# Optimization experiments

Hardware: AMD Instinct MI355X
Metric: run time of the kernel (lower is better)

Reference implementation:

```python
import jax, jax.numpy as jnp
import numpy as np

W_DIM, T_DIM = 300, 100
IN = W_DIM + T_DIM        # 400, also LSTM hidden size
H = IN                    # hiddenSize
BI = 2 * H                # 800, biLSTM output per step
MLP_IN = 2 * BI           # 1600
VOCAB, NTAGS = 50000, 50
SEQ = 320


def _lstm_dir(xs, w_ih, w_hh, b_ih, b_hh, h0, c0, reverse):
    # xs: [T, d_in]; PyTorch gate order i, f, g, o
    if reverse:
        xs = xs[::-1]
    def step(carry, x):
        h, c = carry
        g = x @ w_ih.T + h @ w_hh.T + b_ih + b_hh
        i, f, gc, o = jnp.split(g, 4)
        i, f, o = jax.nn.sigmoid(i), jax.nn.sigmoid(f), jax.nn.sigmoid(o)
        c = f * c + i * jnp.tanh(gc)
        h = o * jnp.tanh(c)
        return (h, c), h
    _, ys = jax.lax.scan(step, (h0, c0), xs)
    return ys[::-1] if reverse else ys


def _bilstm(x, params, h0, c0):
    # x: [T, IN]; h0/c0: [4, H] ordered (l0 fwd, l0 bwd, l1 fwd, l1 bwd)
    out = x
    for layer in range(2):
        p_f = params[layer][0]
        p_b = params[layer][1]
        yf = _lstm_dir(out, *p_f, h0[2 * layer],     c0[2 * layer],     False)
        yb = _lstm_dir(out, *p_b, h0[2 * layer + 1], c0[2 * layer + 1], True)
        out = jnp.concatenate([yf, yb], axis=-1)  # [T, 2H]
    return out


def setup_inputs() -> dict:
    key = jax.random.key(0)
    ks = iter(jax.random.split(key, 32))
    inp = {}
    inp['words'] = jax.random.randint(next(ks), (SEQ,), 0, VOCAB)
    inp['tags'] = jax.random.randint(next(ks), (SEQ,), 0, NTAGS)
    inp['arcs'] = jax.random.randint(next(ks), (SEQ + 1,), 0, SEQ + 1)
    inp['word_emb'] = jax.random.normal(next(ks), (VOCAB, W_DIM), jnp.float32) * 0.1
    inp['tag_emb'] = jax.random.normal(next(ks), (NTAGS, T_DIM), jnp.float32) * 0.1
    inp['h0'] = jax.random.normal(next(ks), (4, H), jnp.float32)
    inp['c0'] = jax.random.normal(next(ks), (4, H), jnp.float32)
    s = 1.0 / np.sqrt(H)
    for layer, d_in in ((0, IN), (1, BI)):
        for suf in ('', 'r'):
            inp[f'w_ih_l{layer}{suf}'] = jax.random.uniform(next(ks), (4 * H, d_in), jnp.float32, -s, s)
            inp[f'w_hh_l{layer}{suf}'] = jax.random.uniform(next(ks), (4 * H, H), jnp.float32, -s, s)
            inp[f'b_ih_l{layer}{suf}'] = jax.random.uniform(next(ks), (4 * H,), jnp.float32, -s, s)
            inp[f'b_hh_l{layer}{suf}'] = jax.random.uniform(next(ks), (4 * H,), jnp.float32, -s, s)
    inp['mlp_w1'] = jax.random.normal(next(ks), (MLP_IN, MLP_IN), jnp.float32) * 0.02
    inp['mlp_b1'] = jnp.zeros((MLP_IN,), jnp.float32)
    inp['mlp_w2'] = jax.random.normal(next(ks), (1, MLP_IN), jnp.float32) * 0.02
    inp['mlp_b2'] = jnp.zeros((1,), jnp.float32)
    return inp


def reference(words, tags, arcs, word_emb, tag_emb, h0, c0,
              w_ih_l0, w_hh_l0, b_ih_l0, b_hh_l0,
              w_ih_l0r, w_hh_l0r, b_ih_l0r, b_hh_l0r,
              w_ih_l1, w_hh_l1, b_ih_l1, b_hh_l1,
              w_ih_l1r, w_hh_l1r, b_ih_l1r, b_hh_l1r,
              mlp_w1, mlp_b1, mlp_w2, mlp_b2):
    n = words.shape[0]
    x = jnp.concatenate([word_emb[words], tag_emb[tags]], axis=1)  # [n, IN]
    params = (((w_ih_l0, w_hh_l0, b_ih_l0, b_hh_l0), (w_ih_l0r, w_hh_l0r, b_ih_l0r, b_hh_l0r)),
              ((w_ih_l1, w_hh_l1, b_ih_l1, b_hh_l1), (w_ih_l1r, w_hh_l1r, b_ih_l1r, b_hh_l1r)))
    hv = _bilstm(x, params, h0, c0)  # [n, BI]
    # pairwise MLP: concat(h_head, h_dep) @ W1.T == h_head @ W1a.T + h_dep @ W1b.T
    w1a, w1b = mlp_w1[:, :BI], mlp_w1[:, BI:]
    a = hv @ w1a.T  # [n, MLP_IN], head part
    b = hv @ w1b.T  # [n, MLP_IN], dep part
    hid = jax.nn.relu(a[:, None, :] + b[None, :, :] + mlp_b1)  # [n, n, MLP_IN]
    scores = jnp.einsum('ndk,ok->nd', hid, mlp_w2)[..., 0] if mlp_w2.shape[0] != 1 else (hid @ mlp_w2[0] + mlp_b2[0])  # [n, n]
    offdiag = 1.0 - jnp.eye(n, dtype=scores.dtype)
    score_tensor = jnp.zeros((n + 1, n + 1), scores.dtype)
    score_tensor = score_tensor.at[0, 0].set(1.0)
    score_tensor = score_tensor.at[1:, 1:].set(scores * offdiag)
    return score_tensor
```

## Files before the change

kernel.cpp:

```cpp
#include <hip/hip_runtime.h>
#include <hip/hip_bf16.h>
#include <hip/hip_fp16.h>

#define SEQ   320
#define GATES 1600
#define NCOL  3200
#define GDW   16
#define RPW   25

typedef _Float16 half2v __attribute__((ext_vector_type(2)));
typedef _Float16 f16x8  __attribute__((ext_vector_type(8)));
typedef float    f32x4  __attribute__((ext_vector_type(4)));
union H2U { unsigned u; half2v h; __half2 hh; };

__global__ __launch_bounds__(256) void prep_kernel(
    const int* __restrict__ words, const int* __restrict__ tags,
    const float* __restrict__ wemb, const float* __restrict__ temb,
    _Float16* __restrict__ Ah0,
    const float* __restrict__ bihl0,  const float* __restrict__ bhhl0,
    const float* __restrict__ bihl0r, const float* __restrict__ bhhl0r,
    const float* __restrict__ bihl1,  const float* __restrict__ bhhl1,
    const float* __restrict__ bihl1r, const float* __restrict__ bhhl1r,
    const float* __restrict__ mlpb1,
    float* __restrict__ bL0, float* __restrict__ bL1, float* __restrict__ bAB,
    const float* __restrict__ wih0, const float* __restrict__ wih0r,
    _Float16* __restrict__ BhA)
{
    const int b = blockIdx.x, t = threadIdx.x;
    if (b < 520) {
        int i = b * 256 + t;
        if (i >= SEQ * 416) return;
        int tt = i / 416, c = i % 416;
        float v = 0.f;
        if (c < 300)      v = wemb[(size_t)words[tt] * 300 + c];
        else if (c < 400) v = temb[(size_t)tags[tt] * 100 + (c - 300)];
        Ah0[i] = (_Float16)v;
    } else if (b < 533) {
        int g = (b - 520) * 256 + t;
        if (g >= NCOL) return;
        if (g < GATES) {
            bL0[g] = bihl0[g] + bhhl0[g];
            bL1[g] = bihl1[g] + bhhl1[g];
            bAB[g] = mlpb1[g];
        } else {
            int q = g - GATES;
            bL0[g] = bihl0r[q] + bhhl0r[q];
            bL1[g] = bihl1r[q] + bhhl1r[q];
            bAB[g] = 0.f;
        }
    } else {
        int i = (b - 533) * 256 + t;
        if (i >= NCOL * 416) return;
        int n = i / 416, k = i % 416;
        float v = 0.f;
        if (k < 400)
            v = (n < GATES) ? wih0[(size_t)n * 400 + k]
                            : wih0r[(size_t)(n - GATES) * 400 + k];
        BhA[i] = (_Float16)v;
    }
}

__global__ __launch_bounds__(256) void cvt2_kernel(
    const float* __restrict__ wih1, const float* __restrict__ wih1r,
    _Float16* __restrict__ BhB,
    const float* __restrict__ mlpw1, _Float16* __restrict__ BhA)
{
    const int b = blockIdx.x, t = threadIdx.x;
    if (b < 10000) {
        int i = b * 256 + t;
        if (i >= NCOL * 800) return;
        int n = i / 800, k = i % 800;
        BhB[i] = (_Float16)((n < GATES) ? wih1[(size_t)n * 800 + k]
                                        : wih1r[(size_t)(n - GATES) * 800 + k]);
    } else {
        int i = (b - 10000) * 256 + t;
        if (i >= NCOL * 800) return;
        int n = i / 800, k = i % 800;
        BhA[i] = (_Float16)((n < GATES) ? mlpw1[(size_t)n * 1600 + k]
                                        : mlpw1[(size_t)(n - GATES) * 1600 + 800 + k]);
    }
}

__global__ __launch_bounds__(256) void gemm_f16(
    const _Float16* __restrict__ A, int Kp,
    const _Float16* __restrict__ B,
    const float* __restrict__ bias, float* __restrict__ C)
{
    const int tid  = threadIdx.x;
    const int w    = tid >> 6, lane = tid & 63;
    const int quad = lane >> 4, l16 = lane & 15;
    const int mb   = blockIdx.y * 32 + (w & 1) * 16;
    const int n0   = blockIdx.x * 64 + (w >> 1) * 32;
    const _Float16* Arow = A + (size_t)(mb + l16) * Kp + quad * 8;
    const _Float16* B0r  = B + (size_t)(n0 + l16) * Kp + quad * 8;
    const _Float16* B1r  = B0r + (size_t)16 * Kp;
    f32x4 acc0 = {0.f, 0.f, 0.f, 0.f}, acc1 = {0.f, 0.f, 0.f, 0.f};
#pragma unroll 4
    for (int k0 = 0; k0 < Kp; k0 += 32) {
        f16x8 a  = *(const f16x8*)(Arow + k0);
        f16x8 b0 = *(const f16x8*)(B0r + k0);
        f16x8 b1 = *(const f16x8*)(B1r + k0);
        acc0 = __builtin_amdgcn_mfma_f32_16x16x32_f16(a, b0, acc0, 0, 0, 0);
        acc1 = __builtin_amdgcn_mfma_f32_16x16x32_f16(a, b1, acc1, 0, 0, 0);
    }
    const int mr = mb + quad * 4;
    float bn0 = bias[n0 + l16], bn1 = bias[n0 + 16 + l16];
#pragma unroll
    for (int r = 0; r < 4; ++r) {
        C[(size_t)(mr + r) * NCOL + n0 + l16]      = acc0[r] + bn0;
        C[(size_t)(mr + r) * NCOL + n0 + 16 + l16] = acc1[r] + bn1;
    }
}

__global__ __launch_bounds__(1024, 4) void lstm_layer(
    const float* __restrict__ gates,
    const float* __restrict__ whh_f, const float* __restrict__ whh_b,
    const float* __restrict__ h0f, const float* __restrict__ h0b,
    const float* __restrict__ c0f, const float* __restrict__ c0b,
    unsigned* __restrict__ ex,
    _Float16* __restrict__ ah)
{
    __shared__ unsigned h_pk[200];
    __shared__ float part[16][28];
    unsigned short* hs = (unsigned short*)h_pk;
    const int tid = threadIdx.x;
    const int dir = blockIdx.x >> 4;
    const int wg  = blockIdx.x & 15;
    const int j0  = wg * RPW;
    const float* whh = dir ? whh_b : whh_f;
    const float* h0d = dir ? h0b : h0f;
    const float* c0d = dir ? c0b : c0f;

    const int w    = tid >> 6;
    const int lane = tid & 63;
    const int g    = w & 3;
    const int kq   = w >> 2;
    const int half = lane & 1;
    const int r    = lane >> 1;
    const int jrow = j0 + (r < RPW ? r : RPW - 1);

    unsigned wr[26];
    {
        const float2* wp = (const float2*)(whh + (size_t)(g * 400 + jrow) * 400 +
                                           kq * 100 + 48 * half);
#pragma unroll
        for (int i = 0; i < 26; ++i) {
            H2U cv; float2 f = wp[i];
            cv.hh = __floats2half2_rn(f.x, f.y);
            wr[i] = (half == 0 && i >= 24) ? 0u : cv.u;
        }
    }

    const int pp = tid / 13;
    const int pd = tid - pp * 13;
    float c_prev = (tid < RPW) ? c0d[j0 + tid] : 0.f;

    for (int s = 0; s < 320; ++s) {
        const int row = dir ? (319 - s) : s;

        float gv0 = 0.f, gv1 = 0.f, gv2 = 0.f, gv3 = 0.f;
        if (tid < RPW) {
            const float* gx = gates + (size_t)row * NCOL + dir * GATES + j0 + tid;
            gv0 = gx[0]; gv1 = gx[400]; gv2 = gx[800]; gv3 = gx[1200];
        }

        if (s == 0) {
            if (tid < 100) {
                float4 f = ((const float4*)h0d)[tid];
                H2U a, b;
                a.hh = __floats2half2_rn(f.x, f.y);
                b.hh = __floats2half2_rn(f.z, f.w);
                ((uint2*)h_pk)[tid] = make_uint2(a.u, b.u);
            }
        } else if (tid < 208 && pp != wg) {
            const int rp = dir ? (row + 1) : (row - 1);
            const unsigned* src = ex + (((size_t)dir * GDW + pp) * SEQ + rp) * 16 + pd;
            unsigned v;
            for (;;) {
                v = __hip_atomic_load(src, __ATOMIC_RELAXED, __HIP_MEMORY_SCOPE_AGENT);
                if ((v & 0xFFFFu) != 0xFFFFu &&
                    (pd == 12 || (v >> 16) != 0xFFFFu)) break;
            }
            const int hb = pp * RPW + pd * 2;
            hs[hb] = (unsigned short)(v & 0xFFFFu);
            if (pd < 12) hs[hb + 1] = (unsigned short)(v >> 16);
        }
        asm volatile("s_waitcnt lgkmcnt(0)" ::: "memory");
        __builtin_amdgcn_s_barrier();

        {
            const uint2* hp2 = (const uint2*)h_pk + kq * 25 + 12 * half;
            float acc = 0.f;
#pragma unroll
            for (int i = 0; i < 13; ++i) {
                uint2 hv2 = hp2[i];
                H2U w0, w1, x0, x1;
                w0.u = wr[2 * i]; w1.u = wr[2 * i + 1];
                x0.u = hv2.x;     x1.u = hv2.y;
                acc = __builtin_amdgcn_fdot2(w0.h, x0.h, acc, false);
                acc = __builtin_amdgcn_fdot2(w1.h, x1.h, acc, false);
            }
            acc += __shfl_xor(acc, 1, 64);
            if (half == 0 && r < RPW) part[w][r] = acc;
        }
        asm volatile("s_waitcnt lgkmcnt(0)" ::: "memory");
        __builtin_amdgcn_s_barrier();

        float hv = 0.f;
        if (tid < RPW) {
            float gi = gv0 + ((part[0][tid] + part[4][tid]) + (part[8][tid]  + part[12][tid]));
            float gf = gv1 + ((part[1][tid] + part[5][tid]) + (part[9][tid]  + part[13][tid]));
            float gg = gv2 + ((part[2][tid] + part[6][tid]) + (part[10][tid] + part[14][tid]));
            float go = gv3 + ((part[3][tid] + part[7][tid]) + (part[11][tid] + part[15][tid]));
            float iv = 1.f / (1.f + __expf(-gi));
            float fv = 1.f / (1.f + __expf(-gf));
            float ov = 1.f / (1.f + __expf(-go));
            float tg = 1.f - 2.f / (1.f + __expf(2.f * gg));
            c_prev = fv * c_prev + iv * tg;
            float tc = 1.f - 2.f / (1.f + __expf(2.f * c_prev));
            hv = ov * tc;
        }
        if (w == 0) {
            int i0 = 2 * lane     < 63 ? 2 * lane     : 63;
            int i1 = 2 * lane + 1 < 63 ? 2 * lane + 1 : 63;
            float xlo = __shfl(hv, i0, 64);
            float xhi = __shfl(hv, i1, 64);
            if (lane < 13) {
                H2U pk;
                pk.hh = __floats2half2_rn(xlo, (2 * lane + 1 < RPW) ? xhi : 0.f);
                __hip_atomic_store(ex + (((size_t)dir * GDW + wg) * SEQ + row) * 16 + lane,
                                   pk.u, __ATOMIC_RELAXED, __HIP_MEMORY_SCOPE_AGENT);
            }
            if (tid < RPW) {
                ah[(size_t)row * 800 + dir * 400 + j0 + tid] = (_Float16)hv;
                H2U o; o.hh = __floats2half2_rn(hv, 0.f);
                hs[RPW * wg + tid] = (unsigned short)(o.u & 0xFFFFu);
            }
        }
    }
}

__global__ __launch_bounds__(256) void scores_kernel(
    const float* __restrict__ ab, const float* __restrict__ w2,
    const float* __restrict__ b2, float* __restrict__ out)
{
    if (blockIdx.y == 20) {
        int i = blockIdx.x * 256 + threadIdx.y * 16 + threadIdx.x;
        if (blockIdx.x < 2 && i < 321) {
            out[i]               = (i == 0) ? 1.f : 0.f;
            out[(size_t)i * 321] = (i == 0) ? 1.f : 0.f;
        }
        return;
    }
    __shared__ float a_s[16 * 132];
    __shared__ float b_s[16 * 132];
    __shared__ float w_s[128];
    const int tx = threadIdx.x, ty = threadIdx.y;
    const int tid = ty * 16 + tx;
    const int n0 = blockIdx.y * 16, d0 = blockIdx.x * 16;
    float acc = 0.f;
    for (int kc = 0; kc < 1600; kc += 128) {
        for (int i = tid; i < 16 * 128; i += 256) {
            int r = i >> 7, c = i & 127;
            a_s[r * 132 + c] = ab[(size_t)(n0 + r) * NCOL + kc + c];
            b_s[r * 132 + c] = ab[(size_t)(d0 + r) * NCOL + 1600 + kc + c];
        }
        if (tid < 128) w_s[tid] = w2[kc + tid];
        __syncthreads();
#pragma unroll
        for (int k = 0; k < 128; k += 4) {
            float4 av = *(const float4*)&a_s[ty * 132 + k];
            float4 bv = *(const float4*)&b_s[tx * 132 + k];
            float4 wv = *(const float4*)&w_s[k];
            acc += fmaxf(av.x + bv.x, 0.f) * wv.x;
            acc += fmaxf(av.y + bv.y, 0.f) * wv.y;
            acc += fmaxf(av.z + bv.z, 0.f) * wv.z;
            acc += fmaxf(av.w + bv.w, 0.f) * wv.w;
        }
        __syncthreads();
    }
    int n = n0 + ty, d = d0 + tx;
    out[(size_t)(n + 1) * 321 + (d + 1)] = (n == d) ? 0.f : (acc + b2[0]);
}

extern "C" void kernel_launch(void* const* d_in, const int* in_sizes, int n_in,
                              void* d_out, int out_size, void* d_ws, size_t ws_size,
                              hipStream_t stream)
{
    const int*   words    = (const int*)d_in[0];
    const int*   tags     = (const int*)d_in[1];
    const float* wemb     = (const float*)d_in[3];
    const float* temb     = (const float*)d_in[4];
    const float* h0       = (const float*)d_in[5];
    const float* c0       = (const float*)d_in[6];
    const float* w_ih_l0  = (const float*)d_in[7];
    const float* w_hh_l0  = (const float*)d_in[8];
    const float* b_ih_l0  = (const float*)d_in[9];
    const float* b_hh_l0  = (const float*)d_in[10];
    const float* w_ih_l0r = (const float*)d_in[11];
    const float* w_hh_l0r = (const float*)d_in[12];
    const float* b_ih_l0r = (const float*)d_in[13];
    const float* b_hh_l0r = (const float*)d_in[14];
    const float* w_ih_l1  = (const float*)d_in[15];
    const float* w_hh_l1  = (const float*)d_in[16];
    const float* b_ih_l1  = (const float*)d_in[17];
    const float* b_hh_l1  = (const float*)d_in[18];
    const float* w_ih_l1r = (const float*)d_in[19];
    const float* w_hh_l1r = (const float*)d_in[20];
    const float* b_ih_l1r = (const float*)d_in[21];
    const float* b_hh_l1r = (const float*)d_in[22];
    const float* mlp_w1   = (const float*)d_in[23];
    const float* mlp_b1   = (const float*)d_in[24];
    const float* mlp_w2   = (const float*)d_in[25];
    const float* mlp_b2   = (const float*)d_in[26];
    float* out = (float*)d_out;

    float* ws      = (float*)d_ws;
    float*    gates  = ws;
    float*    biasL0 = ws + 1024000;
    float*    biasL1 = ws + 1027200;
    float*    biasAB = ws + 1030400;
    unsigned* ex     = (unsigned*)(ws + 1033600);
    _Float16* Ah0    = (_Float16*)(ws + 1361280);
    _Float16* Ah1    = (_Float16*)(ws + 1427840);
    _Float16* Ah2    = (_Float16*)(ws + 1555840);
    _Float16* BhA    = (_Float16*)(ws + 1683840);
    _Float16* BhB    = (_Float16*)(ws + 2963840);
    unsigned* ex0 = ex, *ex1 = ex + 163840;

    hipMemsetAsync(ex, 0xFF, 327680u * 4, stream);

    prep_kernel<<<5733, 256, 0, stream>>>(
        words, tags, wemb, temb, Ah0,
        b_ih_l0, b_hh_l0, b_ih_l0r, b_hh_l0r,
        b_ih_l1, b_hh_l1, b_ih_l1r, b_hh_l1r,
        mlp_b1, biasL0, biasL1, biasAB, w_ih_l0, w_ih_l0r, BhA);

    gemm_f16<<<dim3(50, 10), 256, 0, stream>>>(Ah0, 416, BhA, biasL0, gates);
    cvt2_kernel<<<20000, 256, 0, stream>>>(w_ih_l1, w_ih_l1r, BhB, mlp_w1, BhA);
    lstm_layer<<<2 * GDW, 1024, 0, stream>>>(gates, w_hh_l0, w_hh_l0r,
                                             h0, h0 + 400, c0, c0 + 400, ex0, Ah1);
    gemm_f16<<<dim3(50, 10), 256, 0, stream>>>(Ah1, 800, BhB, biasL1, gates);
    lstm_layer<<<2 * GDW, 1024, 0, stream>>>(gates, w_hh_l1, w_hh_l1r,
                                             h0 + 800, h0 + 1200, c0 + 800, c0 + 1200,
                                             ex1, Ah2);
    gemm_f16<<<dim3(50, 10), 256, 0, stream>>>(Ah2, 800, BhA, biasAB, gates);

    scores_kernel<<<dim3(20, 21), dim3(16, 16), 0, stream>>>(gates, mlp_w2, mlp_b2, out);
}
```

Baseline: 1.373 ms.

## Spread LSTM workgroups across XCDs and double-publish hidden state for faster polling

The LSTM launch grows to 128 blocks, and all but 32 exit at once. The intent is that the surviving blocks (bid&7 < 2) land in a chosen placement across chiplets. Each hidden-state exchange word is now written twice: once by an agent-scope atomic and once by a plain store into a second buffer. Pollers read both copies, using an sc0 load on the second, and accept whichever is ready first. Polling moves off wave 0 onto threads 64-271, and the exchange buffer is re-memset between layers so both copies can reuse it. This costs extra stores, doubled polling traffic, one more memset, and reliance on how the hardware assigns blocks to chiplets.

```diff
diff --git a/kernel.cpp b/kernel.cpp
--- a/kernel.cpp
+++ b/kernel.cpp
@@ -7,6 +7,7 @@
 #define NCOL  3200
 #define GDW   16
 #define RPW   25
+#define EXN   163840
 
 typedef _Float16 half2v __attribute__((ext_vector_type(2)));
 typedef _Float16 f16x8  __attribute__((ext_vector_type(8)));
@@ -120,12 +121,15 @@
     unsigned* __restrict__ ex,
     _Float16* __restrict__ ah)
 {
+    const int bid = blockIdx.x;
+    if ((bid & 7) >= 2) return;
+    const int dir = bid & 7;
+    const int wg  = bid >> 3;
+
     __shared__ unsigned h_pk[200];
     __shared__ float part[16][28];
     unsigned short* hs = (unsigned short*)h_pk;
     const int tid = threadIdx.x;
-    const int dir = blockIdx.x >> 4;
-    const int wg  = blockIdx.x & 15;
     const int j0  = wg * RPW;
     const float* whh = dir ? whh_b : whh_f;
     const float* h0d = dir ? h0b : h0f;
@@ -151,8 +155,9 @@
         }
     }
 
-    const int pp = tid / 13;
-    const int pd = tid - pp * 13;
+    const bool is_poller = (tid >= 64 && tid < 272);
+    const int pp = (tid - 64) / 13;
+    const int pd = (tid - 64) % 13;
     float c_prev = (tid < RPW) ? c0d[j0 + tid] : 0.f;
 
     for (int s = 0; s < 320; ++s) {
@@ -172,14 +177,23 @@
                 b.hh = __floats2half2_rn(f.z, f.w);
                 ((uint2*)h_pk)[tid] = make_uint2(a.u, b.u);
             }
-        } else if (tid < 208 && pp != wg) {
+        } else if (is_poller && pp != wg) {
             const int rp = dir ? (row + 1) : (row - 1);
-            const unsigned* src = ex + (((size_t)dir * GDW + pp) * SEQ + rp) * 16 + pd;
+            const size_t off = (((size_t)dir * GDW + pp) * SEQ + rp) * 16 + pd;
+            const unsigned* srcS = ex + off;
+            const unsigned* srcF = ex + EXN + off;
             unsigned v;
             for (;;) {
-                v = __hip_atomic_load(src, __ATOMIC_RELAXED, __HIP_MEMORY_SCOPE_AGENT);
-                if ((v & 0xFFFFu) != 0xFFFFu &&
-                    (pd == 12 || (v >> 16) != 0xFFFFu)) break;
+                unsigned vs = __hip_atomic_load(srcS, __ATOMIC_RELAXED,
+                                                __HIP_MEMORY_SCOPE_AGENT);
+                unsigned vf;
+                asm volatile("global_load_dword %0, %1, off sc0\n\t"
+                             "s_waitcnt vmcnt(0)"
+                             : "=v"(vf) : "v"(srcF) : "memory");
+                if ((vf & 0xFFFFu) != 0xFFFFu &&
+                    (pd == 12 || (vf >> 16) != 0xFFFFu)) { v = vf; break; }
+                if ((vs & 0xFFFFu) != 0xFFFFu &&
+                    (pd == 12 || (vs >> 16) != 0xFFFFu)) { v = vs; break; }
             }
             const int hb = pp * RPW + pd * 2;
             hs[hb] = (unsigned short)(v & 0xFFFFu);
@@ -228,8 +242,10 @@
             if (lane < 13) {
                 H2U pk;
                 pk.hh = __floats2half2_rn(xlo, (2 * lane + 1 < RPW) ? xhi : 0.f);
-                __hip_atomic_store(ex + (((size_t)dir * GDW + wg) * SEQ + row) * 16 + lane,
-                                   pk.u, __ATOMIC_RELAXED, __HIP_MEMORY_SCOPE_AGENT);
+                const size_t off = (((size_t)dir * GDW + wg) * SEQ + row) * 16 + lane;
+                __hip_atomic_store(ex + off, pk.u,
+                                   __ATOMIC_RELAXED, __HIP_MEMORY_SCOPE_AGENT);
+                ex[EXN + off] = pk.u;
             }
             if (tid < RPW) {
                 ah[(size_t)row * 800 + dir * 400 + j0 + tid] = (_Float16)hv;
@@ -326,7 +342,6 @@
     _Float16* Ah2    = (_Float16*)(ws + 1555840);
     _Float16* BhA    = (_Float16*)(ws + 1683840);
     _Float16* BhB    = (_Float16*)(ws + 2963840);
-    unsigned* ex0 = ex, *ex1 = ex + 163840;
 
     hipMemsetAsync(ex, 0xFF, 327680u * 4, stream);
 
@@ -338,12 +353,13 @@
 
     gemm_f16<<<dim3(50, 10), 256, 0, stream>>>(Ah0, 416, BhA, biasL0, gates);
     cvt2_kernel<<<20000, 256, 0, stream>>>(w_ih_l1, w_ih_l1r, BhB, mlp_w1, BhA);
-    lstm_layer<<<2 * GDW, 1024, 0, stream>>>(gates, w_hh_l0, w_hh_l0r,
-                                             h0, h0 + 400, c0, c0 + 400, ex0, Ah1);
+    lstm_layer<<<128, 1024, 0, stream>>>(gates, w_hh_l0, w_hh_l0r,
+                                         h0, h0 + 400, c0, c0 + 400, ex, Ah1);
+    hipMemsetAsync(ex, 0xFF, 327680u * 4, stream);
     gemm_f16<<<dim3(50, 10), 256, 0, stream>>>(Ah1, 800, BhB, biasL1, gates);
-    lstm_layer<<<2 * GDW, 1024, 0, stream>>>(gates, w_hh_l1, w_hh_l1r,
-                                             h0 + 800, h0 + 1200, c0 + 800, c0 + 1200,
-                                             ex1, Ah2);
+    lstm_layer<<<128, 1024, 0, stream>>>(gates, w_hh_l1, w_hh_l1r,
+                                         h0 + 800, h0 + 1200, c0 + 800, c0 + 1200,
+                                         ex, Ah2);
     gemm_f16<<<dim3(50, 10), 256, 0, stream>>>(Ah2, 800, BhA, biasAB, gates);
 
     scores_kernel<<<dim3(20, 21), dim3(16, 16), 0, stream>>>(gates, mlp_w2, mlp_b2, out);
```

New measurement: 1.272 ms. 7.3% less time.

## Pin each LSTM direction's workgroups to a single XCC via dynamic role assignment

Applied to the files above, without the earlier changes.

The LSTM kernel now launches many surplus workgroups. Each one reads its hardware XCC ID, and a global atomic counter hands out slots so each direction's 16 cooperating workgroups all run on one XCC (XCC 0 forward, XCC 1 backward); the extras exit at once. The aim is to keep the per-step h exchange inside one XCC's L2, cutting cross-die coherence latency. The polling moves to waves 1-4 and uses sc0 loads with a periodic agent-scope fallback, and the writer issues an extra workgroup-scope store. The exchange buffer is reused and re-cleared between layers. It relies on the scheduler spreading blocks so that each of XCC 0 and 1 receives at least 16; if not, the kernel deadlocks, and the launch overhead grows.

```diff
diff --git a/kernel.cpp b/kernel.cpp
--- a/kernel.cpp
+++ b/kernel.cpp
@@ -118,14 +118,29 @@
     const float* __restrict__ h0f, const float* __restrict__ h0b,
     const float* __restrict__ c0f, const float* __restrict__ c0b,
     unsigned* __restrict__ ex,
+    unsigned* __restrict__ cnt,
     _Float16* __restrict__ ah)
 {
     __shared__ unsigned h_pk[200];
     __shared__ float part[16][28];
+    __shared__ int role[2];
     unsigned short* hs = (unsigned short*)h_pk;
     const int tid = threadIdx.x;
-    const int dir = blockIdx.x >> 4;
-    const int wg  = blockIdx.x & 15;
+
+    unsigned xcc;
+    asm volatile("s_getreg_b32 %0, hwreg(HW_REG_XCC_ID)" : "=s"(xcc));
+    if (tid == 0) {
+        int d = (xcc == 0u) ? 0 : (xcc == 1u) ? 1 : -1;
+        int slot = 0x7fffffff;
+        if (d >= 0) slot = (int)atomicAdd(&cnt[d], 1u);
+        role[0] = (d >= 0 && slot < GDW) ? d : -1;
+        role[1] = slot;
+    }
+    __syncthreads();
+    const int dir = role[0];
+    const int wg  = role[1];
+    if (dir < 0) return;
+
     const int j0  = wg * RPW;
     const float* whh = dir ? whh_b : whh_f;
     const float* h0d = dir ? h0b : h0f;
@@ -151,8 +166,6 @@
         }
     }
 
-    const int pp = tid / 13;
-    const int pd = tid - pp * 13;
     float c_prev = (tid < RPW) ? c0d[j0 + tid] : 0.f;
 
     for (int s = 0; s < 320; ++s) {
@@ -172,18 +185,29 @@
                 b.hh = __floats2half2_rn(f.z, f.w);
                 ((uint2*)h_pk)[tid] = make_uint2(a.u, b.u);
             }
-        } else if (tid < 208 && pp != wg) {
-            const int rp = dir ? (row + 1) : (row - 1);
-            const unsigned* src = ex + (((size_t)dir * GDW + pp) * SEQ + rp) * 16 + pd;
-            unsigned v;
-            for (;;) {
-                v = __hip_atomic_load(src, __ATOMIC_RELAXED, __HIP_MEMORY_SCOPE_AGENT);
-                if ((v & 0xFFFFu) != 0xFFFFu &&
-                    (pd == 12 || (v >> 16) != 0xFFFFu)) break;
-            }
-            const int hb = pp * RPW + pd * 2;
-            hs[hb] = (unsigned short)(v & 0xFFFFu);
-            if (pd < 12) hs[hb + 1] = (unsigned short)(v >> 16);
+        } else if (tid >= 64 && tid < 272) {
+            const int idx = tid - 64;
+            const int pp  = idx / 13;
+            const int pd  = idx % 13;
+            if (pp != wg) {
+                const int rp = dir ? (row + 1) : (row - 1);
+                const unsigned* src = ex + (((size_t)dir * GDW + pp) * SEQ + rp) * 16 + pd;
+                unsigned v;
+                for (int it = 0; ; ++it) {
+                    asm volatile("global_load_dword %0, %1, off sc0\n\t"
+                                 "s_waitcnt vmcnt(0)"
+                                 : "=v"(v) : "v"(src) : "memory");
+                    if (v != 0xFFFFFFFFu) break;
+                    if ((it & 15) == 15) {
+                        v = __hip_atomic_load(src, __ATOMIC_RELAXED,
+                                              __HIP_MEMORY_SCOPE_AGENT);
+                        if (v != 0xFFFFFFFFu) break;
+                    }
+                }
+                const int hb = pp * RPW + pd * 2;
+                hs[hb] = (unsigned short)(v & 0xFFFFu);
+                if (pd < 12) hs[hb + 1] = (unsigned short)(v >> 16);
+            }
         }
         asm volatile("s_waitcnt lgkmcnt(0)" ::: "memory");
         __builtin_amdgcn_s_barrier();
@@ -228,8 +252,11 @@
             if (lane < 13) {
                 H2U pk;
                 pk.hh = __floats2half2_rn(xlo, (2 * lane + 1 < RPW) ? xhi : 0.f);
-                __hip_atomic_store(ex + (((size_t)dir * GDW + wg) * SEQ + row) * 16 + lane,
-                                   pk.u, __ATOMIC_RELAXED, __HIP_MEMORY_SCOPE_AGENT);
+                unsigned* dst = ex + (((size_t)dir * GDW + wg) * SEQ + row) * 16 + lane;
+                __hip_atomic_store(dst, pk.u, __ATOMIC_RELAXED,
+                                   __HIP_MEMORY_SCOPE_WORKGROUP);
+                __hip_atomic_store(dst, pk.u, __ATOMIC_RELAXED,
+                                   __HIP_MEMORY_SCOPE_AGENT);
             }
             if (tid < RPW) {
                 ah[(size_t)row * 800 + dir * 400 + j0 + tid] = (_Float16)hv;
@@ -321,14 +348,15 @@
     float*    biasL1 = ws + 1027200;
     float*    biasAB = ws + 1030400;
     unsigned* ex     = (unsigned*)(ws + 1033600);
+    unsigned* cnt    = (unsigned*)(ws + 1197440);
     _Float16* Ah0    = (_Float16*)(ws + 1361280);
     _Float16* Ah1    = (_Float16*)(ws + 1427840);
     _Float16* Ah2    = (_Float16*)(ws + 1555840);
     _Float16* BhA    = (_Float16*)(ws + 1683840);
     _Float16* BhB    = (_Float16*)(ws + 2963840);
-    unsigned* ex0 = ex, *ex1 = ex + 163840;
-
-    hipMemsetAsync(ex, 0xFF, 327680u * 4, stream);
+
+    hipMemsetAsync(ex, 0xFF, 163840u * 4, stream);
+    hipMemsetAsync(cnt, 0, 32, stream);
 
     prep_kernel<<<5733, 256, 0, stream>>>(
         words, tags, wemb, temb, Ah0,
@@ -338,12 +366,14 @@
 
     gemm_f16<<<dim3(50, 10), 256, 0, stream>>>(Ah0, 416, BhA, biasL0, gates);
     cvt2_kernel<<<20000, 256, 0, stream>>>(w_ih_l1, w_ih_l1r, BhB, mlp_w1, BhA);
-    lstm_layer<<<2 * GDW, 1024, 0, stream>>>(gates, w_hh_l0, w_hh_l0r,
-                                             h0, h0 + 400, c0, c0 + 400, ex0, Ah1);
+    lstm_layer<<<512, 1024, 0, stream>>>(gates, w_hh_l0, w_hh_l0r,
+                                         h0, h0 + 400, c0, c0 + 400, ex, cnt, Ah1);
+    hipMemsetAsync(ex, 0xFF, 163840u * 4, stream);
+    hipMemsetAsync(cnt, 0, 32, stream);
     gemm_f16<<<dim3(50, 10), 256, 0, stream>>>(Ah1, 800, BhB, biasL1, gates);
-    lstm_layer<<<2 * GDW, 1024, 0, stream>>>(gates, w_hh_l1, w_hh_l1r,
-                                             h0 + 800, h0 + 1200, c0 + 800, c0 + 1200,
-                                             ex1, Ah2);
+    lstm_layer<<<512, 1024, 0, stream>>>(gates, w_hh_l1, w_hh_l1r,
+                                         h0 + 800, h0 + 1200, c0 + 800, c0 + 1200,
+                                         ex, cnt, Ah2);
     gemm_f16<<<dim3(50, 10), 256, 0, stream>>>(Ah2, 800, BhA, biasAB, gates);
 
     scores_kernel<<<dim3(20, 21), dim3(16, 16), 0, stream>>>(gates, mlp_w2, mlp_b2, out);
```

Measured after the change: 2.363 ms. +72.1%, slower.
